# Performance work log

Hardware: AMD Instinct MI355X
Metric: run time of the kernel (lower is better)

## Reference

```python
import jax, jax.numpy as jnp
import numpy as np

B, S, H = 512, 200, 256

def setup_inputs() -> dict:
    key = jax.random.key(0)
    ks = jax.random.split(key, 7)
    scale = 1.0 / np.sqrt(H)
    return {
        "all_memory": jax.random.normal(ks[0], (B, S, H), dtype=jnp.float32),
        "last_memory": jax.random.normal(ks[1], (B, H), dtype=jnp.float32),
        "U": jax.random.normal(ks[2], (H, H), dtype=jnp.float32) * scale,   # U_meta weight
        "W": jax.random.normal(ks[3], (H, H), dtype=jnp.float32) * scale,   # W_meta weight
        "V": jax.random.normal(ks[4], (H, 1), dtype=jnp.float32) * scale,   # V_meta weight (stored as [H,1])
        "MetaW": jax.random.normal(ks[5], (4, H), dtype=jnp.float32) * scale,  # Meta weight
        "Metab": jax.random.normal(ks[6], (4,), dtype=jnp.float32) * scale,    # Meta bias ('multiple' mode)
    }

def reference(all_memory, last_memory, U, W, V, MetaW, Metab):
    # U_meta(all_memory): [B,S,H]; W_meta(last_memory): [B,H] broadcast over S
    a = jnp.einsum('bsh,kh->bsk', all_memory, U)
    l = jnp.einsum('bh,kh->bk', last_memory, W)
    # additive attention score: V_meta(tanh(a + l)) -> [B,S]
    scores = jnp.einsum('bsh,h->bs', jnp.tanh(a + l[:, None, :]), V[:, 0])
    alpha = jax.nn.softmax(scores, axis=1)  # softmax over seq dim
    pooled = jnp.einsum('bs,bsh->bh', alpha, all_memory)  # weighted sum of values
    return pooled @ MetaW.T + Metab  # [B, 4]
```

## Files before the change

kernel.cpp:

```cpp
#include <hip/hip_runtime.h>
#include <hip/hip_bf16.h>
#include <math.h>

#define NB 512
#define NS 200
#define NH 256
#define TILE_S 32
#define LDSPAD 8
#define LDW (NH + LDSPAD)

#define OFF_L    0
#define OFF_UB   (NB * NH)
#define WS_FLOATS_PRE  (OFF_UB + (NH * NH) / 2)

typedef _Float16 f16x8 __attribute__((ext_vector_type(8)));
typedef float    f32x4 __attribute__((ext_vector_type(4)));

template<int CTRL>
__device__ __forceinline__ float dpp_xadd(float v) {
  return v + __int_as_float(
      __builtin_amdgcn_update_dpp(0, __float_as_int(v), CTRL, 0xf, 0xf, true));
}
__device__ __forceinline__ float row16_sum(float v) {
  v = dpp_xadd<0xB1>(v);
  v = dpp_xadd<0x4E>(v);
  v = dpp_xadd<0x124>(v);
  v = dpp_xadd<0x128>(v);
  return v;
}

__global__ __launch_bounds__(256)
void precompute(const float* __restrict__ lastm, const float* __restrict__ W,
                const float* __restrict__ U,
                float* __restrict__ l_ws, _Float16* __restrict__ Uswz)
{
  const int t = threadIdx.x;
  if (blockIdx.x < NB) {
    const int b = blockIdx.x;
    __shared__ float lm_sm[NH];
    lm_sm[t] = lastm[(size_t)b * NH + t];
    __syncthreads();
    const float4* wrow = (const float4*)(W + (size_t)t * NH);
    const float4* lrow = (const float4*)lm_sm;
    float a0 = 0.f, a1 = 0.f, a2 = 0.f, a3 = 0.f;
#pragma unroll 8
    for (int i = 0; i < NH / 4; ++i) {
      float4 w4 = wrow[i];
      float4 m4 = lrow[i];
      a0 = fmaf(w4.x, m4.x, a0);
      a1 = fmaf(w4.y, m4.y, a1);
      a2 = fmaf(w4.z, m4.z, a2);
      a3 = fmaf(w4.w, m4.w, a3);
    }
    l_ws[(size_t)b * NH + t] = (a0 + a1) + (a2 + a3);
  } else {
    const int id    = (blockIdx.x - NB) * 256 + t;
    const int n_blk = id >> 9;
    const int kk    = (id >> 6) & 7;
    const int lane  = id & 63;
    const int row   = n_blk * 16 + (lane & 15);
    const int col   = kk * 32 + (lane >> 4) * 8;
    const float4* s = (const float4*)(U + (size_t)row * NH + col);
    const float4 a = s[0], c = s[1];
    f16x8 pk;
    pk[0] = (_Float16)a.x; pk[1] = (_Float16)a.y;
    pk[2] = (_Float16)a.z; pk[3] = (_Float16)a.w;
    pk[4] = (_Float16)c.x; pk[5] = (_Float16)c.y;
    pk[6] = (_Float16)c.z; pk[7] = (_Float16)c.w;
    *(f16x8*)(Uswz + (size_t)id * 8) = pk;
  }
}

#define CVT_HL(idx, val) { const float x_ = (val); const _Float16 h_ = (_Float16)x_; \
                           ph[idx] = h_; pl[idx] = (_Float16)(x_ - (float)h_); }

template<bool PRE>
__global__ __launch_bounds__(512, 2)
void fused_attn(const float* __restrict__ mem,
                const float* __restrict__ lastm,
                const float* __restrict__ U,
                const float* __restrict__ W,
                const float* __restrict__ V,
                const float* __restrict__ l_ws,
                const _Float16* __restrict__ Uswz,
                const float* __restrict__ MetaW,
                const float* __restrict__ Metab,
                float* __restrict__ out)
{
  const int b = blockIdx.x;
  const int ntiles = 7;

  const int t     = threadIdx.x;
  const int wave  = t >> 6;
  const int lane  = t & 63;
  const int m16   = lane & 15;
  const int quad  = lane >> 4;
  const int g     = t >> 5;
  const int hblk  = (t & 31) * 8;

  __shared__ __align__(16) _Float16 hi_sm[2][TILE_S][LDW];
  __shared__ __align__(16) _Float16 lo_sm[2][TILE_S][LDW];
  __shared__ float swave_sm[8][TILE_S];
  __shared__ float e_sm[TILE_S];
  __shared__ float z_sm[1];

  float l_reg[2], v_reg[2];
  if constexpr (!PRE) {
    __shared__ float l_sm[NH];
    __shared__ float lm_sm[NH];
    if (t < NH) lm_sm[t] = lastm[(size_t)b * NH + t];
    __syncthreads();
    if (t < NH) {
      const float4* wrow = (const float4*)(W + (size_t)t * NH);
      const float4* lrow = (const float4*)lm_sm;
      float a0 = 0.f, a1 = 0.f, a2 = 0.f, a3 = 0.f;
#pragma unroll 8
      for (int i = 0; i < NH / 4; ++i) {
        float4 w4 = wrow[i];
        float4 m4 = lrow[i];
        a0 = fmaf(w4.x, m4.x, a0);
        a1 = fmaf(w4.y, m4.y, a1);
        a2 = fmaf(w4.z, m4.z, a2);
        a3 = fmaf(w4.w, m4.w, a3);
      }
      l_sm[t] = (a0 + a1) + (a2 + a3);
    }
    __syncthreads();
#pragma unroll
    for (int nf = 0; nf < 2; ++nf)
      l_reg[nf] = l_sm[wave * 32 + nf * 16 + m16];
  } else {
#pragma unroll
    for (int nf = 0; nf < 2; ++nf)
      l_reg[nf] = l_ws[(size_t)b * NH + wave * 32 + nf * 16 + m16];
  }
#pragma unroll
  for (int nf = 0; nf < 2; ++nf)
    v_reg[nf] = V[wave * 32 + nf * 16 + m16];
  const float vsum  = v_reg[0] + v_reg[1];
  const float vm2_0 = -2.f * v_reg[0];
  const float vm2_1 = -2.f * v_reg[1];

  f16x8 u_frag[2][8];
  if constexpr (PRE) {
    const _Float16* uw = Uswz + ((size_t)(wave * 2 * 8 * 64) + lane) * 8;
#pragma unroll
    for (int nf = 0; nf < 2; ++nf)
#pragma unroll
      for (int kk = 0; kk < 8; ++kk)
        u_frag[nf][kk] = *(const f16x8*)(uw + (size_t)((nf * 8 + kk) << 9));
  } else {
#pragma unroll
    for (int nf = 0; nf < 2; ++nf) {
      const int n = wave * 32 + nf * 16 + m16;
      const float* urow = U + (size_t)n * NH;
#pragma unroll
      for (int kk = 0; kk < 8; ++kk) {
        const float4 lo = *(const float4*)(urow + kk * 32 + quad * 8);
        const float4 hi = *(const float4*)(urow + kk * 32 + quad * 8 + 4);
        f16x8 f;
        f[0] = (_Float16)lo.x; f[1] = (_Float16)lo.y;
        f[2] = (_Float16)lo.z; f[3] = (_Float16)lo.w;
        f[4] = (_Float16)hi.x; f[5] = (_Float16)hi.y;
        f[6] = (_Float16)hi.z; f[7] = (_Float16)hi.w;
        u_frag[nf][kk] = f;
      }
    }
  }

  float4 q00, q01, q10, q11;
  {
    const float4* src4 = (const float4*)(mem + (size_t)b * NS * NH);
    const int f0 = t, f1 = 512 + t;
    const float4 a0 = src4[f0 * 2], a1 = src4[f0 * 2 + 1];
    const float4 b0 = src4[f1 * 2], b1 = src4[f1 * 2 + 1];
    {
      f16x8 ph, pl;
      CVT_HL(0, a0.x) CVT_HL(1, a0.y) CVT_HL(2, a0.z) CVT_HL(3, a0.w)
      CVT_HL(4, a1.x) CVT_HL(5, a1.y) CVT_HL(6, a1.z) CVT_HL(7, a1.w)
      *(f16x8*)&hi_sm[0][f0 >> 5][(f0 & 31) * 8] = ph;
      *(f16x8*)&lo_sm[0][f0 >> 5][(f0 & 31) * 8] = pl;
    }
    {
      f16x8 ph, pl;
      CVT_HL(0, b0.x) CVT_HL(1, b0.y) CVT_HL(2, b0.z) CVT_HL(3, b0.w)
      CVT_HL(4, b1.x) CVT_HL(5, b1.y) CVT_HL(6, b1.z) CVT_HL(7, b1.w)
      *(f16x8*)&hi_sm[0][f1 >> 5][(f1 & 31) * 8] = ph;
      *(f16x8*)&lo_sm[0][f1 >> 5][(f1 & 31) * 8] = pl;
    }
    const float4* nsrc = (const float4*)(mem + ((size_t)b * NS + TILE_S) * NH);
    q00 = nsrc[t * 2];         q01 = nsrc[t * 2 + 1];
    q10 = nsrc[(512 + t) * 2]; q11 = nsrc[(512 + t) * 2 + 1];
  }
  __syncthreads();

  float z_local = 0.f;
  float pooledv[8];
#pragma unroll
  for (int j = 0; j < 8; ++j) pooledv[j] = 0.f;

  for (int tile = 0; tile < ntiles; ++tile) {
    const int cur = tile & 1;
    const int nxt = cur ^ 1;
    const int s0  = tile * TILE_S;
    const int rows   = min(TILE_S, NS - s0);
    const int rows_w = (tile + 1 < ntiles) ? min(TILE_S, NS - (s0 + TILE_S)) : 0;
    const int rows_i = (tile + 2 < ntiles) ? min(TILE_S, NS - (s0 + 2 * TILE_S)) : 0;

    f32x4 acc[2][2];
    const f32x4 fzero = {0.f, 0.f, 0.f, 0.f};
#pragma unroll
    for (int mt = 0; mt < 2; ++mt)
#pragma unroll
      for (int nf = 0; nf < 2; ++nf)
        acc[mt][nf] = fzero;

#pragma unroll
    for (int kk = 0; kk < 8; ++kk) {
      const int c = kk * 32 + quad * 8;
      f16x8 a0h = *(const f16x8*)&hi_sm[cur][m16][c];
      f16x8 a1h = *(const f16x8*)&hi_sm[cur][16 + m16][c];
      f16x8 a0l = *(const f16x8*)&lo_sm[cur][m16][c];
      f16x8 a1l = *(const f16x8*)&lo_sm[cur][16 + m16][c];
#pragma unroll
      for (int nf = 0; nf < 2; ++nf) {
        acc[0][nf] = __builtin_amdgcn_mfma_f32_16x16x32_f16(a0h, u_frag[nf][kk], acc[0][nf], 0, 0, 0);
        acc[1][nf] = __builtin_amdgcn_mfma_f32_16x16x32_f16(a1h, u_frag[nf][kk], acc[1][nf], 0, 0, 0);
        acc[0][nf] = __builtin_amdgcn_mfma_f32_16x16x32_f16(a0l, u_frag[nf][kk], acc[0][nf], 0, 0, 0);
        acc[1][nf] = __builtin_amdgcn_mfma_f32_16x16x32_f16(a1l, u_frag[nf][kk], acc[1][nf], 0, 0, 0);
      }
    }

#pragma unroll
    for (int mt = 0; mt < 2; ++mt) {
#pragma unroll
      for (int reg = 0; reg < 4; ++reg) {
        const float x0 = acc[mt][0][reg] + l_reg[0];
        const float x1 = acc[mt][1][reg] + l_reg[1];
        const float e0 = __expf(x0 + x0);
        const float e1 = __expf(x1 + x1);
        float s = vsum;
        s += __fdividef(vm2_0, e0 + 1.f);
        s += __fdividef(vm2_1, e1 + 1.f);
        s = row16_sum(s);
        if (m16 == 0)
          swave_sm[wave][mt * 16 + quad * 4 + reg] = s;
      }
    }
    __syncthreads();

    if (t < TILE_S) {
      float s = swave_sm[0][t];
#pragma unroll
      for (int w = 1; w < 8; ++w) s += swave_sm[w][t];
      const float e = (t < rows) ? __expf(s) : 0.f;
      e_sm[t] = e;
      z_local += e;
    }

    if ((t >> 5) < rows_w) {
      f16x8 ph, pl;
      CVT_HL(0, q00.x) CVT_HL(1, q00.y) CVT_HL(2, q00.z) CVT_HL(3, q00.w)
      CVT_HL(4, q01.x) CVT_HL(5, q01.y) CVT_HL(6, q01.z) CVT_HL(7, q01.w)
      *(f16x8*)&hi_sm[nxt][t >> 5][(t & 31) * 8] = ph;
      *(f16x8*)&lo_sm[nxt][t >> 5][(t & 31) * 8] = pl;
    }
    if (16 + (t >> 5) < rows_w) {
      f16x8 ph, pl;
      CVT_HL(0, q10.x) CVT_HL(1, q10.y) CVT_HL(2, q10.z) CVT_HL(3, q10.w)
      CVT_HL(4, q11.x) CVT_HL(5, q11.y) CVT_HL(6, q11.z) CVT_HL(7, q11.w)
      *(f16x8*)&hi_sm[nxt][16 + (t >> 5)][(t & 31) * 8] = ph;
      *(f16x8*)&lo_sm[nxt][16 + (t >> 5)][(t & 31) * 8] = pl;
    }

    if (rows_i > 0) {
      const float4* nsrc = (const float4*)(mem + ((size_t)b * NS + s0 + 2 * TILE_S) * NH);
      if ((t >> 5) < rows_i)      { q00 = nsrc[t * 2];         q01 = nsrc[t * 2 + 1]; }
      if (16 + (t >> 5) < rows_i) { q10 = nsrc[(512 + t) * 2]; q11 = nsrc[(512 + t) * 2 + 1]; }
    }
    __syncthreads();

    const float e0 = e_sm[2 * g];
    const float e1 = e_sm[2 * g + 1];
    const f16x8 r0 = *(const f16x8*)&hi_sm[cur][2 * g][hblk];
    const f16x8 r1 = *(const f16x8*)&hi_sm[cur][2 * g + 1][hblk];
#pragma unroll
    for (int j = 0; j < 8; ++j)
      pooledv[j] = fmaf(e0, (float)r0[j], fmaf(e1, (float)r1[j], pooledv[j]));
  }
  __syncthreads();

  float* scratch   = (float*)&hi_sm[0][0][0];
  float* pooled_sm = (float*)&lo_sm[0][0][0];
  if (t < TILE_S) {
    float z = z_local;
#pragma unroll
    for (int off = 1; off < 32; off <<= 1)
      z += __shfl_xor(z, off);
    if (t == 0) z_sm[0] = z;
  }
  {
    f32x4 lo4 = {pooledv[0], pooledv[1], pooledv[2], pooledv[3]};
    f32x4 hi4 = {pooledv[4], pooledv[5], pooledv[6], pooledv[7]};
    *(f32x4*)&scratch[g * 264 + hblk]     = lo4;
    *(f32x4*)&scratch[g * 264 + hblk + 4] = hi4;
  }
  __syncthreads();
  const float Zi = 1.f / z_sm[0];
  if (t < NH) {
    float p = 0.f;
#pragma unroll
    for (int r = 0; r < 16; ++r)
      p += scratch[r * 264 + t];
    pooled_sm[t] = p * Zi;
  }
  __syncthreads();
  if (t < 256) {
    float s = 0.f;
#pragma unroll
    for (int i = 0; i < 4; ++i) {
      const int h = i * 64 + lane;
      s = fmaf(pooled_sm[h], MetaW[(size_t)wave * NH + h], s);
    }
#pragma unroll
    for (int off = 32; off > 0; off >>= 1)
      s += __shfl_down(s, off);
    if (lane == 0)
      out[b * 4 + wave] = s + Metab[wave];
  }
}

extern "C" void kernel_launch(void* const* d_in, const int* in_sizes, int n_in,
                              void* d_out, int out_size, void* d_ws, size_t ws_size,
                              hipStream_t stream) {
  const float* mem   = (const float*)d_in[0];
  const float* lastm = (const float*)d_in[1];
  const float* U     = (const float*)d_in[2];
  const float* W     = (const float*)d_in[3];
  const float* V     = (const float*)d_in[4];
  const float* MetaW = (const float*)d_in[5];
  const float* Metab = (const float*)d_in[6];
  float* out = (float*)d_out;
  float* ws  = (float*)d_ws;

  if (ws_size >= (size_t)WS_FLOATS_PRE * sizeof(float)) {
    float*    l_ws = ws + OFF_L;
    _Float16* Uswz = (_Float16*)(ws + OFF_UB);
    hipLaunchKernelGGL(precompute, dim3(NB + 32), dim3(256), 0, stream,
                       lastm, W, U, l_ws, Uswz);
    hipLaunchKernelGGL(fused_attn<true>, dim3(NB), dim3(512), 0, stream,
                       mem, lastm, U, W, V, l_ws, Uswz, MetaW, Metab, out);
  } else {
    hipLaunchKernelGGL(fused_attn<false>, dim3(NB), dim3(512), 0, stream,
                       mem, lastm, U, W, V, (const float*)nullptr, (const _Float16*)nullptr,
                       MetaW, Metab, out);
  }
}
```

Measured before the change: 197.0 us.

## Split each batch's sequence across two blocks and merge partials in a second kernel

```diff
diff --git a/kernel.cpp b/kernel.cpp
--- a/kernel.cpp
+++ b/kernel.cpp
@@ -8,9 +8,12 @@
 #define TILE_S 32
 #define LDSPAD 8
 #define LDW (NH + LDSPAD)
-
-#define OFF_L    0
-#define OFF_UB   (NB * NH)
+#define WS_STRIDE 257
+#define NPART (NB * 2)
+
+#define OFF_PART 0
+#define OFF_L    (NPART * WS_STRIDE)
+#define OFF_UB   (OFF_L + NB * NH)
 #define WS_FLOATS_PRE  (OFF_UB + (NH * NH) / 2)
 
 typedef _Float16 f16x8 __attribute__((ext_vector_type(8)));
@@ -75,20 +78,21 @@
                            ph[idx] = h_; pl[idx] = (_Float16)(x_ - (float)h_); }
 
 template<bool PRE>
-__global__ __launch_bounds__(512, 2)
-void fused_attn(const float* __restrict__ mem,
+__global__ __launch_bounds__(512, 3)
+void fused_part(const float* __restrict__ mem,
                 const float* __restrict__ lastm,
                 const float* __restrict__ U,
                 const float* __restrict__ W,
                 const float* __restrict__ V,
                 const float* __restrict__ l_ws,
                 const _Float16* __restrict__ Uswz,
-                const float* __restrict__ MetaW,
-                const float* __restrict__ Metab,
-                float* __restrict__ out)
+                float* __restrict__ part)
 {
-  const int b = blockIdx.x;
-  const int ntiles = 7;
+  const int b    = blockIdx.x >> 1;
+  const int half = blockIdx.x & 1;
+  const int s_begin = half ? 96 : 0;
+  const int s_end   = half ? NS : 96;
+  const int ntiles  = half ? 4 : 3;
 
   const int t     = threadIdx.x;
   const int wave  = t >> 6;
@@ -99,10 +103,9 @@
   const int hblk  = (t & 31) * 8;
 
   __shared__ __align__(16) _Float16 hi_sm[2][TILE_S][LDW];
-  __shared__ __align__(16) _Float16 lo_sm[2][TILE_S][LDW];
+  __shared__ __align__(16) _Float16 lo_sm[TILE_S][LDW];
   __shared__ float swave_sm[8][TILE_S];
   __shared__ float e_sm[TILE_S];
-  __shared__ float z_sm[1];
 
   float l_reg[2], v_reg[2];
   if constexpr (!PRE) {
@@ -170,7 +173,7 @@
 
   float4 q00, q01, q10, q11;
   {
-    const float4* src4 = (const float4*)(mem + (size_t)b * NS * NH);
+    const float4* src4 = (const float4*)(mem + ((size_t)b * NS + s_begin) * NH);
     const int f0 = t, f1 = 512 + t;
     const float4 a0 = src4[f0 * 2], a1 = src4[f0 * 2 + 1];
     const float4 b0 = src4[f1 * 2], b1 = src4[f1 * 2 + 1];
@@ -179,16 +182,16 @@
       CVT_HL(0, a0.x) CVT_HL(1, a0.y) CVT_HL(2, a0.z) CVT_HL(3, a0.w)
       CVT_HL(4, a1.x) CVT_HL(5, a1.y) CVT_HL(6, a1.z) CVT_HL(7, a1.w)
       *(f16x8*)&hi_sm[0][f0 >> 5][(f0 & 31) * 8] = ph;
-      *(f16x8*)&lo_sm[0][f0 >> 5][(f0 & 31) * 8] = pl;
+      *(f16x8*)&lo_sm[f0 >> 5][(f0 & 31) * 8] = pl;
     }
     {
       f16x8 ph, pl;
       CVT_HL(0, b0.x) CVT_HL(1, b0.y) CVT_HL(2, b0.z) CVT_HL(3, b0.w)
       CVT_HL(4, b1.x) CVT_HL(5, b1.y) CVT_HL(6, b1.z) CVT_HL(7, b1.w)
       *(f16x8*)&hi_sm[0][f1 >> 5][(f1 & 31) * 8] = ph;
-      *(f16x8*)&lo_sm[0][f1 >> 5][(f1 & 31) * 8] = pl;
-    }
-    const float4* nsrc = (const float4*)(mem + ((size_t)b * NS + TILE_S) * NH);
+      *(f16x8*)&lo_sm[f1 >> 5][(f1 & 31) * 8] = pl;
+    }
+    const float4* nsrc = (const float4*)(mem + ((size_t)b * NS + s_begin + TILE_S) * NH);
     q00 = nsrc[t * 2];         q01 = nsrc[t * 2 + 1];
     q10 = nsrc[(512 + t) * 2]; q11 = nsrc[(512 + t) * 2 + 1];
   }
@@ -202,10 +205,10 @@
   for (int tile = 0; tile < ntiles; ++tile) {
     const int cur = tile & 1;
     const int nxt = cur ^ 1;
-    const int s0  = tile * TILE_S;
-    const int rows   = min(TILE_S, NS - s0);
-    const int rows_w = (tile + 1 < ntiles) ? min(TILE_S, NS - (s0 + TILE_S)) : 0;
-    const int rows_i = (tile + 2 < ntiles) ? min(TILE_S, NS - (s0 + 2 * TILE_S)) : 0;
+    const int s0  = s_begin + tile * TILE_S;
+    const int rows   = min(TILE_S, s_end - s0);
+    const int rows_w = (tile + 1 < ntiles) ? min(TILE_S, s_end - (s0 + TILE_S)) : 0;
+    const int rows_i = (tile + 2 < ntiles) ? min(TILE_S, s_end - (s0 + 2 * TILE_S)) : 0;
 
     f32x4 acc[2][2];
     const f32x4 fzero = {0.f, 0.f, 0.f, 0.f};
@@ -220,8 +223,8 @@
       const int c = kk * 32 + quad * 8;
       f16x8 a0h = *(const f16x8*)&hi_sm[cur][m16][c];
       f16x8 a1h = *(const f16x8*)&hi_sm[cur][16 + m16][c];
-      f16x8 a0l = *(const f16x8*)&lo_sm[cur][m16][c];
-      f16x8 a1l = *(const f16x8*)&lo_sm[cur][16 + m16][c];
+      f16x8 a0l = *(const f16x8*)&lo_sm[m16][c];
+      f16x8 a1l = *(const f16x8*)&lo_sm[16 + m16][c];
 #pragma unroll
       for (int nf = 0; nf < 2; ++nf) {
         acc[0][nf] = __builtin_amdgcn_mfma_f32_16x16x32_f16(a0h, u_frag[nf][kk], acc[0][nf], 0, 0, 0);
@@ -263,14 +266,14 @@
       CVT_HL(0, q00.x) CVT_HL(1, q00.y) CVT_HL(2, q00.z) CVT_HL(3, q00.w)
       CVT_HL(4, q01.x) CVT_HL(5, q01.y) CVT_HL(6, q01.z) CVT_HL(7, q01.w)
       *(f16x8*)&hi_sm[nxt][t >> 5][(t & 31) * 8] = ph;
-      *(f16x8*)&lo_sm[nxt][t >> 5][(t & 31) * 8] = pl;
+      *(f16x8*)&lo_sm[t >> 5][(t & 31) * 8] = pl;
     }
     if (16 + (t >> 5) < rows_w) {
       f16x8 ph, pl;
       CVT_HL(0, q10.x) CVT_HL(1, q10.y) CVT_HL(2, q10.z) CVT_HL(3, q10.w)
       CVT_HL(4, q11.x) CVT_HL(5, q11.y) CVT_HL(6, q11.z) CVT_HL(7, q11.w)
       *(f16x8*)&hi_sm[nxt][16 + (t >> 5)][(t & 31) * 8] = ph;
-      *(f16x8*)&lo_sm[nxt][16 + (t >> 5)][(t & 31) * 8] = pl;
+      *(f16x8*)&lo_sm[16 + (t >> 5)][(t & 31) * 8] = pl;
     }
 
     if (rows_i > 0) {
@@ -290,14 +293,14 @@
   }
   __syncthreads();
 
-  float* scratch   = (float*)&hi_sm[0][0][0];
-  float* pooled_sm = (float*)&lo_sm[0][0][0];
+  float* base    = part + (size_t)blockIdx.x * WS_STRIDE;
+  float* scratch = (float*)&hi_sm[0][0][0];
   if (t < TILE_S) {
     float z = z_local;
 #pragma unroll
     for (int off = 1; off < 32; off <<= 1)
       z += __shfl_xor(z, off);
-    if (t == 0) z_sm[0] = z;
+    if (t == 0) base[0] = z;
   }
   {
     f32x4 lo4 = {pooledv[0], pooledv[1], pooledv[2], pooledv[3]};
@@ -306,28 +309,45 @@
     *(f32x4*)&scratch[g * 264 + hblk + 4] = hi4;
   }
   __syncthreads();
-  const float Zi = 1.f / z_sm[0];
   if (t < NH) {
     float p = 0.f;
 #pragma unroll
     for (int r = 0; r < 16; ++r)
       p += scratch[r * 264 + t];
-    pooled_sm[t] = p * Zi;
-  }
+    base[1 + t] = p;
+  }
+}
+
+__global__ __launch_bounds__(256)
+void merge_project(const float* __restrict__ part,
+                   const float* __restrict__ MetaW,
+                   const float* __restrict__ Metab,
+                   float* __restrict__ out)
+{
+  const int b    = blockIdx.x;
+  const int t    = threadIdx.x;
+  const int wave = t >> 6;
+  const int lane = t & 63;
+
+  __shared__ float pooled_sm[NH];
+
+  const float* b0 = part + (size_t)(b * 2)     * WS_STRIDE;
+  const float* b1 = part + (size_t)(b * 2 + 1) * WS_STRIDE;
+  const float Zi = 1.f / (b0[0] + b1[0]);
+  pooled_sm[t] = (b0[1 + t] + b1[1 + t]) * Zi;
   __syncthreads();
-  if (t < 256) {
-    float s = 0.f;
-#pragma unroll
-    for (int i = 0; i < 4; ++i) {
-      const int h = i * 64 + lane;
-      s = fmaf(pooled_sm[h], MetaW[(size_t)wave * NH + h], s);
-    }
-#pragma unroll
-    for (int off = 32; off > 0; off >>= 1)
-      s += __shfl_down(s, off);
-    if (lane == 0)
-      out[b * 4 + wave] = s + Metab[wave];
-  }
+
+  float s = 0.f;
+#pragma unroll
+  for (int i = 0; i < 4; ++i) {
+    const int h = i * 64 + lane;
+    s = fmaf(pooled_sm[h], MetaW[(size_t)wave * NH + h], s);
+  }
+#pragma unroll
+  for (int off = 32; off > 0; off >>= 1)
+    s += __shfl_down(s, off);
+  if (lane == 0)
+    out[b * 4 + wave] = s + Metab[wave];
 }
 
 extern "C" void kernel_launch(void* const* d_in, const int* in_sizes, int n_in,
@@ -343,16 +363,20 @@
   float* out = (float*)d_out;
   float* ws  = (float*)d_ws;
 
+  float* part = ws + OFF_PART;
+
   if (ws_size >= (size_t)WS_FLOATS_PRE * sizeof(float)) {
     float*    l_ws = ws + OFF_L;
     _Float16* Uswz = (_Float16*)(ws + OFF_UB);
     hipLaunchKernelGGL(precompute, dim3(NB + 32), dim3(256), 0, stream,
                        lastm, W, U, l_ws, Uswz);
-    hipLaunchKernelGGL(fused_attn<true>, dim3(NB), dim3(512), 0, stream,
-                       mem, lastm, U, W, V, l_ws, Uswz, MetaW, Metab, out);
+    hipLaunchKernelGGL(fused_part<true>, dim3(NPART), dim3(512), 0, stream,
+                       mem, lastm, U, W, V, l_ws, Uswz, part);
   } else {
-    hipLaunchKernelGGL(fused_attn<false>, dim3(NB), dim3(512), 0, stream,
+    hipLaunchKernelGGL(fused_part<false>, dim3(NPART), dim3(512), 0, stream,
                        mem, lastm, U, W, V, (const float*)nullptr, (const _Float16*)nullptr,
-                       MetaW, Metab, out);
-  }
-}
+                       part);
+  }
+  hipLaunchKernelGGL(merge_project, dim3(NB), dim3(256), 0, stream,
+                     part, MetaW, Metab, out);
+}
```

Result: slower. 210.3 us (+6.7%).
